# Kernel optimization log

Measured on AMD Instinct MI355X. Metric: run time of the kernel, lower is better.

Reference implementation:

```python
import jax, jax.numpy as jnp
import numpy as np

E, H = 8, 32  # num_experts, hidden_size


def _experts_mlp(x, W1, b1, W2, b2):
    """Run all tiny experts densely on x: x [N,1] -> [E, N, 1]."""
    h = jax.nn.relu(jnp.einsum('ni,eih->enh', x, W1) + b1[:, None, :])  # [E,N,H]
    return jnp.einsum('enh,eho->eno', h, W2) + b2[:, None, :]           # [E,N,1]


def setup_inputs() -> dict:
    key = jax.random.key(0)
    k_ctx, k_in, k1, k2, k3, k4 = jax.random.split(key, 6)
    B = 131072
    context = jax.random.normal(k_ctx, (B, 8), dtype=jnp.float32)
    inp = jax.random.normal(k_in, (B, 1), dtype=jnp.float32)
    # Expert params (Linear(1->32), ReLU, Linear(32->1)) stacked over experts.
    W1 = jax.random.normal(k1, (E, 1, H), dtype=jnp.float32) / np.sqrt(1.0)
    b1 = jax.random.normal(k2, (E, H), dtype=jnp.float32) * 0.1
    W2 = jax.random.normal(k3, (E, H, 1), dtype=jnp.float32) / np.sqrt(H)
    b2 = jax.random.normal(k4, (E, 1), dtype=jnp.float32) * 0.1
    return {"context": context, "input": inp, "W1": W1, "b1": b1, "W2": W2, "b2": b2}


def reference(context, input, W1, b1, W2, b2):
    B = context.shape[0]
    P = context.shape[1] // 2  # = 4 context (x,y) pairs
    context_x = context[:, 0::2].reshape(-1, 1)  # [B*P, 1]
    context_y = context[:, 1::2].reshape(-1, 1)  # [B*P, 1]
    # Per-expert predictions on context x-values.
    preds = _experts_mlp(context_x, W1, b1, W2, b2)          # [E, B*P, 1]
    err = (preds - context_y[None]).reshape(E, B, P)         # [E, B, P]
    error_context = jnp.sum(err * err, axis=2).T             # [B, E]
    weights = jax.nn.softmax(-error_context, axis=1)         # [B, E]
    expert_outputs = _experts_mlp(input, W1, b1, W2, b2)     # [E, B, 1]
    expert_outputs = jnp.transpose(expert_outputs, (1, 0, 2))  # [B, E, 1]
    combined = jnp.sum(weights[:, :, None] * expert_outputs, axis=1)  # [B, 1]
    return combined
```

## Files before the change

kernel.cpp:

```cpp
#include <hip/hip_runtime.h>


constexpr int E = 8;
constexpr int H = 32;
constexpr int STRIDE = 34;

__global__ __launch_bounds__(256) void moe_kernel(
    const float* __restrict__ ctx,
    const float* __restrict__ inp,
    const float* __restrict__ W1,
    const float* __restrict__ b1,
    const float* __restrict__ W2,
    const float* __restrict__ b2,
    float* __restrict__ out,
    int B)
{
    __shared__ __align__(16) float2 crs[E * STRIDE];

    const int t = threadIdx.x;
    {
        const int e = t >> 5;
        const int h = t & 31;
        const float w1  = W1[e * H + h];
        const float b1v = b1[e * H + h];
        const float w2  = W2[e * H + h];
        const float aw  = fabsf(w1);
        const bool tiny = aw < 1e-20f;
        const float c = tiny ? 0.f : 0.5f * w2 * aw;
        const float r = tiny ? 0.f : (-b1v / w1);
        float pa = tiny ? 0.f : 0.5f * w2 * w1;
        float pb = tiny ? (w2 * fmaxf(b1v, 0.f)) : (0.5f * w2 * b1v);

        crs[e * STRIDE + h] = make_float2(c, r);

        #pragma unroll
        for (int m = 1; m < 32; m <<= 1) {
            pa += __shfl_xor(pa, m);
            pb += __shfl_xor(pb, m);
        }
        if (h == 0) {
            const float beta = pb + b2[e];
            crs[e * STRIDE + 32] = make_float2(pa, -16.0f);
            crs[e * STRIDE + 33] = make_float2(beta - 16.0f * pa, 0.f);
        }
    }
    __syncthreads();

    const int g = blockIdx.x * 256 + t;
    const int b = g >> 3;
    const int e = g & 7;
    if (b >= B) return;

    const float4 c0 = reinterpret_cast<const float4*>(ctx)[b * 2 + 0];
    const float4 c1 = reinterpret_cast<const float4*>(ctx)[b * 2 + 1];
    const float x4 = inp[b];

    float4 crq[17];
    const float4* __restrict__ rowp =
        reinterpret_cast<const float4*>(&crs[e * STRIDE]);
    #pragma unroll
    for (int i = 0; i < 17; ++i) crq[i] = rowp[i];

    const float K = crq[16].z;
    float a0 = K, a1 = K, a2 = K, a3 = K, a4 = K;

    #pragma unroll
    for (int i = 0; i < 16; ++i) {
        {
            const float c = crq[i].x, r = crq[i].y;
            a0 = fmaf(c, fabsf(c0.x - r), a0);
            a1 = fmaf(c, fabsf(c0.z - r), a1);
            a2 = fmaf(c, fabsf(c1.x - r), a2);
            a3 = fmaf(c, fabsf(c1.z - r), a3);
            a4 = fmaf(c, fabsf(x4  - r), a4);
        }
        {
            const float c = crq[i].z, r = crq[i].w;
            a0 = fmaf(c, fabsf(c0.x - r), a0);
            a1 = fmaf(c, fabsf(c0.z - r), a1);
            a2 = fmaf(c, fabsf(c1.x - r), a2);
            a3 = fmaf(c, fabsf(c1.z - r), a3);
            a4 = fmaf(c, fabsf(x4  - r), a4);
        }
    }
    {
        const float c = crq[16].x, r = crq[16].y;
        a0 = fmaf(c, fabsf(c0.x - r), a0);
        a1 = fmaf(c, fabsf(c0.z - r), a1);
        a2 = fmaf(c, fabsf(c1.x - r), a2);
        a3 = fmaf(c, fabsf(c1.z - r), a3);
        a4 = fmaf(c, fabsf(x4  - r), a4);
    }

    const float p0 = a0 - c0.y;
    const float p1 = a1 - c0.w;
    const float p2 = a2 - c1.y;
    const float p3 = a3 - c1.w;
    const float err = fmaf(p0, p0, fmaf(p1, p1, fmaf(p2, p2, p3 * p3)));
    const float oe  = a4;

    float m = err;
    m = fminf(m, __shfl_xor(m, 1));
    m = fminf(m, __shfl_xor(m, 2));
    m = fminf(m, __shfl_xor(m, 4));
    const float w = __expf(m - err);
    float s  = w;
    float wo = w * oe;
    s  += __shfl_xor(s, 1);  wo += __shfl_xor(wo, 1);
    s  += __shfl_xor(s, 2);  wo += __shfl_xor(wo, 2);
    s  += __shfl_xor(s, 4);  wo += __shfl_xor(wo, 4);

    if (e == 0) out[b] = wo / s;
}

extern "C" void kernel_launch(void* const* d_in, const int* in_sizes, int n_in,
                              void* d_out, int out_size, void* d_ws, size_t ws_size,
                              hipStream_t stream) {
    const float* ctx = (const float*)d_in[0];
    const float* inp = (const float*)d_in[1];
    const float* W1  = (const float*)d_in[2];
    const float* b1  = (const float*)d_in[3];
    const float* W2  = (const float*)d_in[4];
    const float* b2  = (const float*)d_in[5];
    float* out = (float*)d_out;

    const int B = in_sizes[1];
    const long long total = (long long)B * 8;
    const int threads = 256;
    const int blocks = (int)((total + threads - 1) / threads);
    hipLaunchKernelGGL(moe_kernel, dim3(blocks), dim3(threads), 0, stream,
                       ctx, inp, W1, b1, W2, b2, out, B);
}
```

Before: 15.15 us.

## Use persistent grid-stride loop with software-prefetched context loads

The kernel now launches at most 1024 blocks and has each thread loop over several (batch, expert) items with a grid stride. The per-block shared-memory setup (expert coefficient table plus shuffle reductions) is amortized across iterations. The next iteration's context and input values are loaded before the current compute so memory latency overlaps with ALU work. The trade is fewer resident waves for latency hiding and extra registers for the prefetch buffers.

After: 15.74 us. 3.9% more time.

```diff
diff --git a/kernel.cpp b/kernel.cpp
--- a/kernel.cpp
+++ b/kernel.cpp
@@ -46,71 +46,90 @@
     }
     __syncthreads();
 
-    const int g = blockIdx.x * 256 + t;
-    const int b = g >> 3;
+    const int total  = B * 8;
+    const int stride = (int)gridDim.x * 256;
+    int g = (int)blockIdx.x * 256 + t;
+    if (g >= total) return;
     const int e = g & 7;
-    if (b >= B) return;
-
-    const float4 c0 = reinterpret_cast<const float4*>(ctx)[b * 2 + 0];
-    const float4 c1 = reinterpret_cast<const float4*>(ctx)[b * 2 + 1];
-    const float x4 = inp[b];
 
     float4 crq[17];
     const float4* __restrict__ rowp =
         reinterpret_cast<const float4*>(&crs[e * STRIDE]);
     #pragma unroll
     for (int i = 0; i < 17; ++i) crq[i] = rowp[i];
+    const float K = crq[16].z;
 
-    const float K = crq[16].z;
-    float a0 = K, a1 = K, a2 = K, a3 = K, a4 = K;
+    const float4* __restrict__ ctxq = reinterpret_cast<const float4*>(ctx);
 
-    #pragma unroll
-    for (int i = 0; i < 16; ++i) {
+    int b = g >> 3;
+    float4 c0 = ctxq[b * 2 + 0];
+    float4 c1 = ctxq[b * 2 + 1];
+    float x4 = inp[b];
+
+    while (true) {
+        const int gn = g + stride;
+        const bool more = gn < total;
+        float4 n0, n1; float n4;
+        if (more) {
+            const int bn = gn >> 3;
+            n0 = ctxq[bn * 2 + 0];
+            n1 = ctxq[bn * 2 + 1];
+            n4 = inp[bn];
+        }
+
+        float a0 = K, a1 = K, a2 = K, a3 = K, a4 = K;
+        #pragma unroll
+        for (int i = 0; i < 16; ++i) {
+            {
+                const float c = crq[i].x, r = crq[i].y;
+                a0 = fmaf(c, fabsf(c0.x - r), a0);
+                a1 = fmaf(c, fabsf(c0.z - r), a1);
+                a2 = fmaf(c, fabsf(c1.x - r), a2);
+                a3 = fmaf(c, fabsf(c1.z - r), a3);
+                a4 = fmaf(c, fabsf(x4  - r), a4);
+            }
+            {
+                const float c = crq[i].z, r = crq[i].w;
+                a0 = fmaf(c, fabsf(c0.x - r), a0);
+                a1 = fmaf(c, fabsf(c0.z - r), a1);
+                a2 = fmaf(c, fabsf(c1.x - r), a2);
+                a3 = fmaf(c, fabsf(c1.z - r), a3);
+                a4 = fmaf(c, fabsf(x4  - r), a4);
+            }
+        }
         {
-            const float c = crq[i].x, r = crq[i].y;
+            const float c = crq[16].x, r = crq[16].y;
             a0 = fmaf(c, fabsf(c0.x - r), a0);
             a1 = fmaf(c, fabsf(c0.z - r), a1);
             a2 = fmaf(c, fabsf(c1.x - r), a2);
             a3 = fmaf(c, fabsf(c1.z - r), a3);
             a4 = fmaf(c, fabsf(x4  - r), a4);
         }
-        {
-            const float c = crq[i].z, r = crq[i].w;
-            a0 = fmaf(c, fabsf(c0.x - r), a0);
-            a1 = fmaf(c, fabsf(c0.z - r), a1);
-            a2 = fmaf(c, fabsf(c1.x - r), a2);
-            a3 = fmaf(c, fabsf(c1.z - r), a3);
-            a4 = fmaf(c, fabsf(x4  - r), a4);
-        }
+
+        const float p0 = a0 - c0.y;
+        const float p1 = a1 - c0.w;
+        const float p2 = a2 - c1.y;
+        const float p3 = a3 - c1.w;
+        const float err = fmaf(p0, p0, fmaf(p1, p1, fmaf(p2, p2, p3 * p3)));
+        const float oe  = a4;
+
+        float m = err;
+        m = fminf(m, __shfl_xor(m, 1));
+        m = fminf(m, __shfl_xor(m, 2));
+        m = fminf(m, __shfl_xor(m, 4));
+        const float w = __expf(m - err);
+        float s  = w;
+        float wo = w * oe;
+        s  += __shfl_xor(s, 1);  wo += __shfl_xor(wo, 1);
+        s  += __shfl_xor(s, 2);  wo += __shfl_xor(wo, 2);
+        s  += __shfl_xor(s, 4);  wo += __shfl_xor(wo, 4);
+
+        if (e == 0) out[g >> 3] = wo / s;
+
+        if (!more) break;
+        g = gn;
+        c0 = n0; c1 = n1; x4 = n4;
     }
-    {
-        const float c = crq[16].x, r = crq[16].y;
-        a0 = fmaf(c, fabsf(c0.x - r), a0);
-        a1 = fmaf(c, fabsf(c0.z - r), a1);
-        a2 = fmaf(c, fabsf(c1.x - r), a2);
-        a3 = fmaf(c, fabsf(c1.z - r), a3);
-        a4 = fmaf(c, fabsf(x4  - r), a4);
-    }
-
-    const float p0 = a0 - c0.y;
-    const float p1 = a1 - c0.w;
-    const float p2 = a2 - c1.y;
-    const float p3 = a3 - c1.w;
-    const float err = fmaf(p0, p0, fmaf(p1, p1, fmaf(p2, p2, p3 * p3)));
-    const float oe  = a4;
-
-    float m = err;
-    m = fminf(m, __shfl_xor(m, 1));
-    m = fminf(m, __shfl_xor(m, 2));
-    m = fminf(m, __shfl_xor(m, 4));
-    const float w = __expf(m - err);
-    float s  = w;
-    float wo = w * oe;
-    s  += __shfl_xor(s, 1);  wo += __shfl_xor(wo, 1);
-    s  += __shfl_xor(s, 2);  wo += __shfl_xor(wo, 2);
-    s  += __shfl_xor(s, 4);  wo += __shfl_xor(wo, 4);
-
-    if (e == 0) out[b] = wo / s;
 }
 
 extern "C" void kernel_launch(void* const* d_in, const int* in_sizes, int n_in,
@@ -126,8 +145,8 @@
 
     const int B = in_sizes[1];
     const long long total = (long long)B * 8;
-    const int threads = 256;
-    const int blocks = (int)((total + threads - 1) / threads);
-    hipLaunchKernelGGL(moe_kernel, dim3(blocks), dim3(threads), 0, stream,
+    int blocks = (int)((total + 255) / 256);
+    if (blocks > 1024) blocks = 1024;
+    hipLaunchKernelGGL(moe_kernel, dim3(blocks), dim3(256), 0, stream,
                        ctx, inp, W1, b1, W2, b2, out, B);
 }
```
